# Kernel tuning notes

Hardware: AMD Instinct MI355X
Metric: run time of the kernel (lower is better)

Reference implementation:

```python
import jax, jax.numpy as jnp
import numpy as np

N_TRAIN, N_FEAT, N_HID, ENC = 4096, 64, 256, 256
N_ANTES, ATT_H, MAX_LEN = 2048, 256, 16


def setup_inputs() -> dict:
    key = jax.random.key(0)
    ks = jax.random.split(key, 8)
    s = 0.05
    f32 = jnp.float32
    return {
        "context": jax.random.normal(ks[0], (N_TRAIN, N_FEAT), f32),
        "S": jax.random.uniform(ks[1], (N_TRAIN, N_ANTES), dtype=f32),
        "enc_w1": s * jax.random.normal(ks[2], (N_HID, N_FEAT), f32),
        "enc_b1": jnp.zeros((N_HID,), f32),
        "enc_w2": s * jax.random.normal(ks[3], (ENC, N_HID), f32),
        "enc_b2": jnp.zeros((ENC,), f32),
        "w_ih": s * jax.random.normal(ks[4], (4 * ENC, N_ANTES), f32),
        "w_hh": s * jax.random.normal(ks[5], (4 * ENC, ENC), f32),
        "b_ih": jnp.zeros((4 * ENC,), f32),
        "b_hh": jnp.zeros((4 * ENC,), f32),
        "att_w1": s * jax.random.normal(ks[6], (ATT_H, N_TRAIN + ENC), f32),
        "att_b1": jnp.zeros((ATT_H,), f32),
        "att_w2": s * jax.random.normal(ks[7], (1, ATT_H), f32),
        "att_b2": jnp.zeros((1,), f32),
    }


def _forward(context, S, enc_w1, enc_b1, enc_w2, enc_b2,
             w_ih, w_hh, b_ih, b_hh, att_w1, att_b1, att_w2, att_b2):
    n_train, n_antes = S.shape
    # context encoder: Linear -> ReLU -> Linear, initializes LSTM hidden state
    phi = jax.nn.relu(context @ enc_w1.T + enc_b1) @ enc_w2.T + enc_b2  # [n_train, ENC]
    # attention first layer split: columns [:n_train] act on S.T rows, rest on e_t
    Wa, Wb = att_w1[:, :n_train], att_w1[:, n_train:]
    pre = S.T @ Wa.T  # [n_antes, ATT_H], constant across timesteps
    bias = b_ih + b_hh
    x0 = jnp.ones((n_train, n_antes), S.dtype)

    def step(carry, _):
        h, c, x = carry
        # one LSTM cell step (PyTorch gate order i, f, g, o)
        z = x @ w_ih.T + h @ w_hh.T + bias  # [n_train, 4*ENC]
        i, f, g, o = jnp.split(z, 4, axis=-1)
        c = jax.nn.sigmoid(f) * c + jax.nn.sigmoid(i) * jnp.tanh(g)
        h = jax.nn.sigmoid(o) * jnp.tanh(c)
        e_t = h.mean(axis=0)  # mean over n_train (torch e.mean(1) on [1,n_train,H])
        hid = jax.nn.relu(pre + e_t @ Wb.T + att_b1)  # [n_antes, ATT_H]
        scores = (hid @ att_w2.T + att_b2)[:, 0]      # [n_antes]
        logp = jax.nn.log_softmax(scores, axis=0)
        idx = jnp.argmax(logp)
        # next input: chosen antecedent column broadcast across all antecedents
        x_next = jnp.broadcast_to(S[:, idx][:, None], (n_train, n_antes))
        return (h, c, x_next), logp

    _, d = jax.lax.scan(jax.checkpoint(step), (phi, jnp.zeros_like(phi), x0),
                        None, length=MAX_LEN)
    return d  # [MAX_LEN, n_antes] == torch cat(...).transpose(0, 1)


def reference(context, S, enc_w1, enc_b1, enc_w2, enc_b2,
              w_ih, w_hh, b_ih, b_hh, att_w1, att_b1, att_w2, att_b2):
    return _forward(context, S, enc_w1, enc_b1, enc_w2, enc_b2,
                    w_ih, w_hh, b_ih, b_hh, att_w1, att_b1, att_w2, att_b2)
```

## Files before the change

kernel.cpp:

```cpp
#include <hip/hip_runtime.h>
#include <hip/hip_bf16.h>
#include <math.h>

#define N_TRAIN 4096
#define N_FEAT  64
#define N_HID   256
#define ENC     256
#define N_ANTES 2048
#define ATT_H   256
#define MAX_LEN 16

typedef unsigned int u32;
typedef unsigned short u16;
typedef short short8 __attribute__((ext_vector_type(8)));
typedef float floatx16 __attribute__((ext_vector_type(16)));

__device__ __forceinline__ float fsig(float x)  { return 1.f / (1.f + __expf(-x)); }
__device__ __forceinline__ float ftanh(float x) { return 2.f / (1.f + __expf(-2.f * x)) - 1.f; }

__device__ __forceinline__ u16 f2bf(float x) {
    u32 b = __float_as_uint(x);
    return (u16)((b + 0x7FFFu + ((b >> 16) & 1u)) >> 16);
}
__device__ __forceinline__ float bf2f(u16 h) {
    return __uint_as_float(((u32)h) << 16);
}

__device__ __forceinline__ int kin_of(int l, int j) {
    return ((l >> 5) << 2) + (j & 3) + ((j >> 2) << 3);
}

template <bool RELU>
__global__ __launch_bounds__(256) void gemm_abT(
    const float* __restrict__ A, const float* __restrict__ B,
    const float* __restrict__ bias, float* __restrict__ C,
    int M, int N, int K, int lda, int ldb, int ldc)
{
    __shared__ __align__(16) float As[16][68];
    __shared__ __align__(16) float Bs[16][68];
    const int tid = threadIdx.x;
    const int m0 = blockIdx.x * 64, n0 = blockIdx.y * 64;
    const int tx = tid & 15, ty = tid >> 4;
    const int kl = tid & 15, rl = tid >> 4;
    float acc[4][4] = {};

    for (int k0 = 0; k0 < K; k0 += 16) {
        #pragma unroll
        for (int pp = 0; pp < 4; ++pp) {
            int r = rl + pp * 16;
            As[kl][r] = A[(size_t)(m0 + r) * lda + k0 + kl];
            Bs[kl][r] = B[(size_t)(n0 + r) * ldb + k0 + kl];
        }
        __syncthreads();
        #pragma unroll
        for (int k = 0; k < 16; ++k) {
            float4 av = *(const float4*)&As[k][ty * 4];
            float4 bv = *(const float4*)&Bs[k][tx * 4];
            float a4[4] = {av.x, av.y, av.z, av.w};
            float b4[4] = {bv.x, bv.y, bv.z, bv.w};
            #pragma unroll
            for (int i = 0; i < 4; ++i)
                #pragma unroll
                for (int j = 0; j < 4; ++j)
                    acc[i][j] = fmaf(a4[i], b4[j], acc[i][j]);
        }
        __syncthreads();
    }
    #pragma unroll
    for (int i = 0; i < 4; ++i) {
        int m = m0 + ty * 4 + i;
        #pragma unroll
        for (int j = 0; j < 4; ++j) {
            int n = n0 + tx * 4 + j;
            float v = acc[i][j] + bias[n];
            if (RELU) v = fmaxf(v, 0.f);
            C[(size_t)m * ldc + n] = v;
        }
    }
}

#define KSPLIT 8
__global__ __launch_bounds__(256) void gemm_ab_splitk(
    const float* __restrict__ A, const float* __restrict__ B,
    float* __restrict__ P0, float* __restrict__ P1, float* __restrict__ P2,
    int M, int N, int K, int lda, int ldb, int ldc)
{
    __shared__ __align__(16) float As[16][68];
    __shared__ __align__(16) float Bs[16][64];
    const int tid = threadIdx.x;
    const int m0 = blockIdx.x * 64, n0 = blockIdx.y * 64;
    const int kchunk = K / KSPLIT;
    const int kbeg = blockIdx.z * kchunk, kend = kbeg + kchunk;
    const int tx = tid & 15, ty = tid >> 4;
    const int kl = tid & 15, rl = tid >> 4;
    const int kb = tid >> 6, nb = tid & 63;
    float acc[4][4] = {};

    for (int k0 = kbeg; k0 < kend; k0 += 16) {
        #pragma unroll
        for (int pp = 0; pp < 4; ++pp) {
            As[kl][rl + pp * 16] = A[(size_t)(m0 + rl + pp * 16) * lda + k0 + kl];
            Bs[kb + pp * 4][nb]  = B[(size_t)(k0 + kb + pp * 4) * ldb + n0 + nb];
        }
        __syncthreads();
        #pragma unroll
        for (int k = 0; k < 16; ++k) {
            float4 av = *(const float4*)&As[k][ty * 4];
            float4 bv = *(const float4*)&Bs[k][tx * 4];
            float a4[4] = {av.x, av.y, av.z, av.w};
            float b4[4] = {bv.x, bv.y, bv.z, bv.w};
            #pragma unroll
            for (int i = 0; i < 4; ++i)
                #pragma unroll
                for (int j = 0; j < 4; ++j)
                    acc[i][j] = fmaf(a4[i], b4[j], acc[i][j]);
        }
        __syncthreads();
    }
    const int SZ = ATT_H * N_ANTES;
    const int bz = blockIdx.z;
    float* Cp = (bz < 4) ? P0 + (size_t)bz * SZ
              : (bz < 6) ? P1 + (size_t)(bz - 4) * SZ
                         : P2 + (size_t)(bz - 6) * SZ;
    #pragma unroll
    for (int i = 0; i < 4; ++i)
        #pragma unroll
        for (int j = 0; j < 4; ++j)
            Cp[(size_t)(m0 + ty * 4 + i) * ldc + n0 + tx * 4 + j] = acc[i][j];
}

__global__ __launch_bounds__(256) void k_reduce(
    const float* __restrict__ P0, const float* __restrict__ P1,
    const float* __restrict__ P2, float* __restrict__ preT)
{
    int gid = blockIdx.x * 256 + threadIdx.x;
    const int SZ = ATT_H * N_ANTES;
    float s = ((P0[gid] + P0[gid + SZ]) + (P0[gid + 2 * SZ] + P0[gid + 3 * SZ]))
            + ((P1[gid] + P1[gid + SZ]) + (P2[gid] + P2[gid + SZ]));
    preT[gid] = s;
}

__global__ __launch_bounds__(256) void k_rowsum(const float* __restrict__ w_ih,
                                                float* __restrict__ rowsum)
{
    __shared__ float red[256];
    const int j = blockIdx.x, tid = threadIdx.x;
    float s = 0.f;
    for (int i = tid; i < N_ANTES; i += 256) s += w_ih[(size_t)j * N_ANTES + i];
    red[tid] = s; __syncthreads();
    for (int off = 128; off > 0; off >>= 1) {
        if (tid < off) red[tid] += red[tid + off];
        __syncthreads();
    }
    if (tid == 0) rowsum[j] = red[0];
}

__global__ __launch_bounds__(256) void k_wbT(const float* __restrict__ att_w1,
                                             float* __restrict__ WbT)
{
    int gid = blockIdx.x * 256 + threadIdx.x;
    int j = gid >> 8, k = gid & 255;
    WbT[(size_t)k * 256 + j] = att_w1[(size_t)j * (N_TRAIN + ENC) + N_TRAIN + k];
}

__global__ __launch_bounds__(256) void k_packWf(const float* __restrict__ w_hh,
                                                u16* __restrict__ Wf_hi,
                                                u16* __restrict__ Wf_lo)
{
    int gid = blockIdx.x * 256 + threadIdx.x;
    int j    = gid & 7;
    int l    = (gid >> 3) & 63;
    int kt   = (gid >> 9) & 15;
    int nsub = (gid >> 13) & 1;
    int cb   = gid >> 14;
    int k  = kt * 16 + kin_of(l, j);
    int cc = nsub * 32 + (l & 31);
    int jj = cb * 16 + (cc >> 2);
    int g  = cc & 3;
    int J  = g * 256 + jj;
    float v = w_hh[(size_t)J * 256 + k];
    u16 hi = f2bf(v);
    Wf_hi[gid] = hi;
    Wf_lo[gid] = f2bf(v - bf2f(hi));
}

__global__ __launch_bounds__(256) void k_packHf(const float* __restrict__ h,
                                                u16* __restrict__ Hf_hi,
                                                u16* __restrict__ Hf_lo)
{
    int gid = blockIdx.x * 256 + threadIdx.x;
    int j  = gid & 7;
    int l  = (gid >> 3) & 63;
    int kt = (gid >> 9) & 15;
    int mt = gid >> 13;
    int m = mt * 32 + (l & 31);
    int k = kt * 16 + kin_of(l, j);
    float v = h[(size_t)m * 256 + k];
    u16 hi = f2bf(v);
    Hf_hi[gid] = hi;
    Hf_lo[gid] = f2bf(v - bf2f(hi));
}

__global__ __launch_bounds__(256) void k_zgemm(
    const u16* __restrict__ Hf_hi_r, const u16* __restrict__ Hf_lo_r,
    u16* __restrict__ Hf_hi_w, u16* __restrict__ Hf_lo_w,
    const u16* __restrict__ Wf_hi, const u16* __restrict__ Wf_lo,
    float* __restrict__ c,
    const float* __restrict__ rowsum, const float* __restrict__ b_ih,
    const float* __restrict__ b_hh, const float* __restrict__ S,
    const int* __restrict__ idx_buf, int t, float* __restrict__ e_acc_t)
{
    __shared__ __align__(16) float z_lds[128][68];
    __shared__ float red[256];
    const int tid  = threadIdx.x;
    const int lane = tid & 63;
    const int msub = tid >> 6;
    const int rb = blockIdx.x;
    const int cb = blockIdx.y;
    const int mt = rb * 4 + msub;

    floatx16 acc0 = {0,0,0,0,0,0,0,0,0,0,0,0,0,0,0,0};
    floatx16 acc1 = {0,0,0,0,0,0,0,0,0,0,0,0,0,0,0,0};
    const size_t aoff  = (size_t)mt * 16 * 512 + lane * 8;
    const size_t boff0 = (size_t)(cb * 2 + 0) * 16 * 512 + lane * 8;
    const size_t boff1 = (size_t)(cb * 2 + 1) * 16 * 512 + lane * 8;

    #pragma unroll 4
    for (int kt = 0; kt < 16; ++kt) {
        short8 ahi = *(const short8*)(Hf_hi_r + aoff  + kt * 512);
        short8 alo = *(const short8*)(Hf_lo_r + aoff  + kt * 512);
        short8 b0h = *(const short8*)(Wf_hi   + boff0 + kt * 512);
        short8 b0l = *(const short8*)(Wf_lo   + boff0 + kt * 512);
        short8 b1h = *(const short8*)(Wf_hi   + boff1 + kt * 512);
        short8 b1l = *(const short8*)(Wf_lo   + boff1 + kt * 512);
        acc0 = __builtin_amdgcn_mfma_f32_32x32x16_bf16(ahi, b0h, acc0, 0, 0, 0);
        acc0 = __builtin_amdgcn_mfma_f32_32x32x16_bf16(ahi, b0l, acc0, 0, 0, 0);
        acc0 = __builtin_amdgcn_mfma_f32_32x32x16_bf16(alo, b0h, acc0, 0, 0, 0);
        acc1 = __builtin_amdgcn_mfma_f32_32x32x16_bf16(ahi, b1h, acc1, 0, 0, 0);
        acc1 = __builtin_amdgcn_mfma_f32_32x32x16_bf16(ahi, b1l, acc1, 0, 0, 0);
        acc1 = __builtin_amdgcn_mfma_f32_32x32x16_bf16(alo, b1h, acc1, 0, 0, 0);
    }

    #pragma unroll
    for (int q = 0; q < 16; ++q) {
        int row = msub * 32 + (q & 3) + 8 * (q >> 2) + 4 * (lane >> 5);
        z_lds[row][lane & 31]        = acc0[q];
        z_lds[row][32 + (lane & 31)] = acc1[q];
    }
    __syncthreads();

    const int jj_l = tid & 15, rg = tid >> 4;
    const int Jc = cb * 16 + jj_l;
    float rs[4], bs[4];
    #pragma unroll
    for (int g = 0; g < 4; ++g) {
        int J = g * 256 + Jc;
        rs[g] = rowsum[J];
        bs[g] = b_ih[J] + b_hh[J];
    }
    const int idxp = (t > 0) ? idx_buf[t - 1] : 0;
    float esum = 0.f;
    #pragma unroll
    for (int p = 0; p < 8; ++p) {
        int r = rg * 8 + p;
        int rglob = rb * 128 + r;
        float a = (t > 0) ? S[(size_t)rglob * N_ANTES + idxp] : 1.f;
        float4 z4 = *(const float4*)&z_lds[r][jj_l * 4];
        float zi = z4.x + fmaf(a, rs[0], bs[0]);
        float zf = z4.y + fmaf(a, rs[1], bs[1]);
        float zg = z4.z + fmaf(a, rs[2], bs[2]);
        float zo = z4.w + fmaf(a, rs[3], bs[3]);
        size_t coff = (size_t)rglob * 256 + Jc;
        float cn = fsig(zf) * c[coff] + fsig(zi) * ftanh(zg);
        float hn = fsig(zo) * ftanh(cn);
        c[coff] = cn;
        esum += hn;
        u16 hi = f2bf(hn);
        u16 lo = f2bf(hn - bf2f(hi));
        int mtw    = rglob >> 5;
        int lane_a = (rglob & 31) + 32 * ((Jc >> 2) & 1);
        int ktw    = Jc >> 4;
        int jw     = (Jc & 3) + ((Jc >> 3) & 1) * 4;
        size_t off = (((size_t)mtw * 16 + ktw) * 64 + lane_a) * 8 + jw;
        Hf_hi_w[off] = hi;
        Hf_lo_w[off] = lo;
    }
    red[tid] = esum;
    __syncthreads();
    if (tid < 16) {
        float s = 0.f;
        #pragma unroll
        for (int q = 0; q < 16; ++q) s += red[tid + q * 16];
        atomicAdd(&e_acc_t[Jc - jj_l + tid], s);
    }
}

__global__ __launch_bounds__(256) void k_att(
    const float* __restrict__ preT, const float* __restrict__ e_accum_t,
    const float* __restrict__ WbT, const float* __restrict__ att_b1,
    const float* __restrict__ att_w2, const float* __restrict__ att_b2,
    float* __restrict__ scores, float* __restrict__ out_t,
    int* __restrict__ idx_t, int* __restrict__ cnt)
{
    __shared__ float e_lds[256];
    __shared__ float u[256];
    __shared__ float w2s[256];
    __shared__ float red[256];
    const int tid = threadIdx.x;
    e_lds[tid] = e_accum_t[tid] * (1.f / (float)N_TRAIN);
    w2s[tid] = att_w2[tid];
    __syncthreads();

    float uacc = att_b1[tid];
    for (int k = 0; k < 256; ++k)
        uacc = fmaf(e_lds[k], WbT[(size_t)k * 256 + tid], uacc);
    u[tid] = uacc;
    __syncthreads();

    const int pl = tid & 31, jq = tid >> 5;
    const int p = blockIdx.x * 32 + pl;
    float sc = 0.f;
    #pragma unroll 4
    for (int j = jq; j < 256; j += 8) {
        float v = preT[(size_t)j * N_ANTES + p] + u[j];
        sc = fmaf(fmaxf(v, 0.f), w2s[j], sc);
    }
    red[tid] = sc;
    __syncthreads();
    if (tid < 32) {
        float s = att_b2[0];
        #pragma unroll
        for (int q = 0; q < 8; ++q) s += red[tid + q * 32];
        scores[blockIdx.x * 32 + tid] = s;
    }

    __threadfence();
    __syncthreads();
    __shared__ int is_last;
    if (tid == 0)
        is_last = (atomicAdd(cnt, 1) == (int)gridDim.x - 1);
    __syncthreads();
    if (!is_last) return;
    __threadfence();

    __shared__ float smax[256];
    __shared__ int   sidx[256];
    __shared__ float ssum[256];

    float sv[8];
    #pragma unroll
    for (int i = 0; i < 8; ++i) sv[i] = scores[tid * 8 + i];

    float lmax = -INFINITY; int lidx = 0;
    #pragma unroll
    for (int i = 0; i < 8; ++i)
        if (sv[i] > lmax) { lmax = sv[i]; lidx = tid * 8 + i; }
    smax[tid] = lmax; sidx[tid] = lidx;
    __syncthreads();
    for (int off = 128; off > 0; off >>= 1) {
        if (tid < off) {
            float ov = smax[tid + off]; int oi = sidx[tid + off];
            if (ov > smax[tid] || (ov == smax[tid] && oi < sidx[tid])) {
                smax[tid] = ov; sidx[tid] = oi;
            }
        }
        __syncthreads();
    }
    const float gmax = smax[0];
    const int gidx = sidx[0];

    float lsum = 0.f;
    #pragma unroll
    for (int i = 0; i < 8; ++i) lsum += __expf(sv[i] - gmax);
    ssum[tid] = lsum;
    __syncthreads();
    for (int off = 128; off > 0; off >>= 1) {
        if (tid < off) ssum[tid] += ssum[tid + off];
        __syncthreads();
    }
    const float lse = gmax + logf(ssum[0]);

    #pragma unroll
    for (int i = 0; i < 8; ++i)
        out_t[tid * 8 + i] = sv[i] - lse;
    if (tid == 0) {
        idx_t[0] = gidx;
        *cnt = 0;
    }
}

extern "C" void kernel_launch(void* const* d_in, const int* in_sizes, int n_in,
                              void* d_out, int out_size, void* d_ws, size_t ws_size,
                              hipStream_t stream)
{
    (void)in_sizes; (void)n_in; (void)out_size; (void)ws_size;
    const float* context = (const float*)d_in[0];
    const float* S       = (const float*)d_in[1];
    const float* enc_w1  = (const float*)d_in[2];
    const float* enc_b1  = (const float*)d_in[3];
    const float* enc_w2  = (const float*)d_in[4];
    const float* enc_b2  = (const float*)d_in[5];
    const float* w_ih    = (const float*)d_in[6];
    const float* w_hh    = (const float*)d_in[7];
    const float* b_ih    = (const float*)d_in[8];
    const float* b_hh    = (const float*)d_in[9];
    const float* att_w1  = (const float*)d_in[10];
    const float* att_b1  = (const float*)d_in[11];
    const float* att_w2  = (const float*)d_in[12];
    const float* att_b2  = (const float*)d_in[13];
    float* out = (float*)d_out;
    float* ws  = (float*)d_ws;

    float* h_fp32 = ws;
    float* c      = ws + 1048576;
    float* hid1   = ws + 2097152;
    float* preT   = ws + 3145728;
    float* P2     = ws + 3670016;
    u16* Hf_hi1 = (u16*)(ws + 0);
    u16* Hf_lo1 = (u16*)(ws + 524288);
    u16* Hf_hi0 = (u16*)(ws + 2097152);
    u16* Hf_lo0 = (u16*)(ws + 2621440);
    u16* Wf_hi  = (u16*)(ws + 3670016);
    u16* Wf_lo  = (u16*)(ws + 3801088);
    int*   cnt    = (int*)(ws + 4718592);
    float* rowsum = ws + 4984832;
    float* e_acc  = ws + 4985856;
    float* scores = ws + 4989952;
    float* WbT    = ws + 4992000;
    int*   idxbuf = (int*)(ws + 5057536);

    k_rowsum<<<1024, 256, 0, stream>>>(w_ih, rowsum);
    k_wbT<<<256, 256, 0, stream>>>(att_w1, WbT);

    dim3 g3(ATT_H / 64, N_ANTES / 64, KSPLIT);
    gemm_ab_splitk<<<g3, 256, 0, stream>>>(att_w1, S, ws, hid1, P2,
                                           ATT_H, N_ANTES, N_TRAIN,
                                           N_TRAIN + ENC, N_ANTES, N_ANTES);
    k_reduce<<<(ATT_H * N_ANTES) / 256, 256, 0, stream>>>(ws, hid1, P2, preT);

    k_packWf<<<1024, 256, 0, stream>>>(w_hh, Wf_hi, Wf_lo);
    hipMemsetAsync(c, 0, (size_t)N_TRAIN * ENC * sizeof(float), stream);
    hipMemsetAsync(e_acc, 0, (size_t)MAX_LEN * ENC * sizeof(float), stream);
    hipMemsetAsync(cnt, 0, sizeof(int), stream);

    dim3 g1(N_TRAIN / 64, N_HID / 64);
    gemm_abT<true><<<g1, 256, 0, stream>>>(context, enc_w1, enc_b1, hid1,
                                           N_TRAIN, N_HID, N_FEAT, N_FEAT, N_FEAT, N_HID);
    dim3 g2(N_TRAIN / 64, ENC / 64);
    gemm_abT<false><<<g2, 256, 0, stream>>>(hid1, enc_w2, enc_b2, h_fp32,
                                            N_TRAIN, ENC, N_HID, N_HID, N_HID, ENC);
    k_packHf<<<4096, 256, 0, stream>>>(h_fp32, Hf_hi0, Hf_lo0);

    dim3 gz(32, 16);
    for (int t = 0; t < MAX_LEN; ++t) {
        const u16 *hr, *lr; u16 *hw, *lw;
        if ((t & 1) == 0) { hr = Hf_hi0; lr = Hf_lo0; hw = Hf_hi1; lw = Hf_lo1; }
        else              { hr = Hf_hi1; lr = Hf_lo1; hw = Hf_hi0; lw = Hf_lo0; }
        k_zgemm<<<gz, 256, 0, stream>>>(hr, lr, hw, lw, Wf_hi, Wf_lo, c,
                                        rowsum, b_ih, b_hh, S, idxbuf, t,
                                        e_acc + t * 256);
        k_att<<<N_ANTES / 32, 256, 0, stream>>>(preT, e_acc + t * 256, WbT,
                                                att_b1, att_w2, att_b2, scores,
                                                out + t * N_ANTES, idxbuf + t, cnt);
    }
}
```

Baseline: 725.3 us.

## Compute attention precompute GEMM with split-bf16 MFMA instead of FP32 split-K

Replaces the FP32 SIMT split-K GEMM for pre = att_w1[:, :n_train] @ S with an MFMA kernel that uses a 3-term bf16 hi/lo split to keep roughly FP32 accuracy. att_w1 is pre-packed into the MFMA fragment layout, and S is split on the fly. The split-K factor drops from 8 to 4, so the reduce kernel reads fewer partials. It adds a pack kernel and strided global reads of S without LDS staging, and the hi/lo split is a truncation-based approximation of FP32.

```diff
diff --git a/kernel.cpp b/kernel.cpp
--- a/kernel.cpp
+++ b/kernel.cpp
@@ -24,6 +24,12 @@
 }
 __device__ __forceinline__ float bf2f(u16 h) {
     return __uint_as_float(((u32)h) << 16);
+}
+__device__ __forceinline__ void split_bf(float v, u16& hi, u16& lo) {
+    u32 b = __float_as_uint(v);
+    hi = (u16)(b >> 16);
+    float r = v - __uint_as_float(b & 0xFFFF0000u);
+    lo = (u16)(__float_as_uint(r) >> 16);
 }
 
 __device__ __forceinline__ int kin_of(int l, int j) {
@@ -79,67 +85,6 @@
     }
 }
 
-#define KSPLIT 8
-__global__ __launch_bounds__(256) void gemm_ab_splitk(
-    const float* __restrict__ A, const float* __restrict__ B,
-    float* __restrict__ P0, float* __restrict__ P1, float* __restrict__ P2,
-    int M, int N, int K, int lda, int ldb, int ldc)
-{
-    __shared__ __align__(16) float As[16][68];
-    __shared__ __align__(16) float Bs[16][64];
-    const int tid = threadIdx.x;
-    const int m0 = blockIdx.x * 64, n0 = blockIdx.y * 64;
-    const int kchunk = K / KSPLIT;
-    const int kbeg = blockIdx.z * kchunk, kend = kbeg + kchunk;
-    const int tx = tid & 15, ty = tid >> 4;
-    const int kl = tid & 15, rl = tid >> 4;
-    const int kb = tid >> 6, nb = tid & 63;
-    float acc[4][4] = {};
-
-    for (int k0 = kbeg; k0 < kend; k0 += 16) {
-        #pragma unroll
-        for (int pp = 0; pp < 4; ++pp) {
-            As[kl][rl + pp * 16] = A[(size_t)(m0 + rl + pp * 16) * lda + k0 + kl];
-            Bs[kb + pp * 4][nb]  = B[(size_t)(k0 + kb + pp * 4) * ldb + n0 + nb];
-        }
-        __syncthreads();
-        #pragma unroll
-        for (int k = 0; k < 16; ++k) {
-            float4 av = *(const float4*)&As[k][ty * 4];
-            float4 bv = *(const float4*)&Bs[k][tx * 4];
-            float a4[4] = {av.x, av.y, av.z, av.w};
-            float b4[4] = {bv.x, bv.y, bv.z, bv.w};
-            #pragma unroll
-            for (int i = 0; i < 4; ++i)
-                #pragma unroll
-                for (int j = 0; j < 4; ++j)
-                    acc[i][j] = fmaf(a4[i], b4[j], acc[i][j]);
-        }
-        __syncthreads();
-    }
-    const int SZ = ATT_H * N_ANTES;
-    const int bz = blockIdx.z;
-    float* Cp = (bz < 4) ? P0 + (size_t)bz * SZ
-              : (bz < 6) ? P1 + (size_t)(bz - 4) * SZ
-                         : P2 + (size_t)(bz - 6) * SZ;
-    #pragma unroll
-    for (int i = 0; i < 4; ++i)
-        #pragma unroll
-        for (int j = 0; j < 4; ++j)
-            Cp[(size_t)(m0 + ty * 4 + i) * ldc + n0 + tx * 4 + j] = acc[i][j];
-}
-
-__global__ __launch_bounds__(256) void k_reduce(
-    const float* __restrict__ P0, const float* __restrict__ P1,
-    const float* __restrict__ P2, float* __restrict__ preT)
-{
-    int gid = blockIdx.x * 256 + threadIdx.x;
-    const int SZ = ATT_H * N_ANTES;
-    float s = ((P0[gid] + P0[gid + SZ]) + (P0[gid + 2 * SZ] + P0[gid + 3 * SZ]))
-            + ((P1[gid] + P1[gid + SZ]) + (P2[gid] + P2[gid + SZ]));
-    preT[gid] = s;
-}
-
 __global__ __launch_bounds__(256) void k_rowsum(const float* __restrict__ w_ih,
                                                 float* __restrict__ rowsum)
 {
@@ -161,6 +106,90 @@
     int gid = blockIdx.x * 256 + threadIdx.x;
     int j = gid >> 8, k = gid & 255;
     WbT[(size_t)k * 256 + j] = att_w1[(size_t)j * (N_TRAIN + ENC) + N_TRAIN + k];
+}
+
+__global__ __launch_bounds__(256) void k_packAf(const float* __restrict__ att_w1,
+                                                u16* __restrict__ Af_hi,
+                                                u16* __restrict__ Af_lo)
+{
+    int gid = blockIdx.x * 256 + threadIdx.x;
+    int j  = gid & 7;
+    int l  = (gid >> 3) & 63;
+    int kt = (gid >> 9) & 255;
+    int mt = gid >> 17;
+    int m = mt * 32 + (l & 31);
+    int k = kt * 16 + kin_of(l, j);
+    float v = att_w1[(size_t)m * (N_TRAIN + ENC) + k];
+    u16 hi, lo; split_bf(v, hi, lo);
+    Af_hi[gid] = hi;
+    Af_lo[gid] = lo;
+}
+
+#define PSPLIT 4
+__global__ __launch_bounds__(256) void k_gemm_preT(
+    const u16* __restrict__ Af_hi, const u16* __restrict__ Af_lo,
+    const float* __restrict__ S, float* __restrict__ P)
+{
+    const int tid = threadIdx.x, lane = tid & 63, w = tid >> 6;
+    const int kz = blockIdx.x;
+    const int np = blockIdx.y;
+    const int p0 = np * 64;
+    const int nb = p0 + (lane & 31);
+    const int kb = 4 * (lane >> 5);
+    floatx16 acc[2][2] = {};
+
+    const int kt_beg = kz * 64, kt_end = kt_beg + 64;
+    #pragma unroll 2
+    for (int kt = kt_beg; kt < kt_end; ++kt) {
+        short8 ahi[2], alo[2], bhi[2], blo[2];
+        #pragma unroll
+        for (int mi = 0; mi < 2; ++mi) {
+            size_t ao = (((size_t)(w * 2 + mi) * 256 + kt) * 64 + lane) * 8;
+            ahi[mi] = *(const short8*)(Af_hi + ao);
+            alo[mi] = *(const short8*)(Af_lo + ao);
+        }
+        #pragma unroll
+        for (int ni = 0; ni < 2; ++ni) {
+            #pragma unroll
+            for (int j = 0; j < 8; ++j) {
+                int k = kt * 16 + kb + (j & 3) + 8 * (j >> 2);
+                float v = S[(size_t)k * N_ANTES + nb + ni * 32];
+                u16 hi, lo; split_bf(v, hi, lo);
+                bhi[ni][j] = (short)hi;
+                blo[ni][j] = (short)lo;
+            }
+        }
+        #pragma unroll
+        for (int mi = 0; mi < 2; ++mi)
+            #pragma unroll
+            for (int ni = 0; ni < 2; ++ni) {
+                acc[mi][ni] = __builtin_amdgcn_mfma_f32_32x32x16_bf16(
+                    ahi[mi], bhi[ni], acc[mi][ni], 0, 0, 0);
+                acc[mi][ni] = __builtin_amdgcn_mfma_f32_32x32x16_bf16(
+                    ahi[mi], blo[ni], acc[mi][ni], 0, 0, 0);
+                acc[mi][ni] = __builtin_amdgcn_mfma_f32_32x32x16_bf16(
+                    alo[mi], bhi[ni], acc[mi][ni], 0, 0, 0);
+            }
+    }
+
+    float* Pk = P + (size_t)kz * (ATT_H * N_ANTES);
+    #pragma unroll
+    for (int mi = 0; mi < 2; ++mi)
+        #pragma unroll
+        for (int ni = 0; ni < 2; ++ni)
+            #pragma unroll
+            for (int q = 0; q < 16; ++q) {
+                int row = w * 64 + mi * 32 + (q & 3) + 8 * (q >> 2) + 4 * (lane >> 5);
+                Pk[(size_t)row * N_ANTES + p0 + ni * 32 + (lane & 31)] = acc[mi][ni][q];
+            }
+}
+
+__global__ __launch_bounds__(256) void k_reduce4(const float* __restrict__ P,
+                                                 float* __restrict__ preT)
+{
+    int gid = blockIdx.x * 256 + threadIdx.x;
+    const int SZ = ATT_H * N_ANTES;
+    preT[gid] = (P[gid] + P[gid + SZ]) + (P[gid + 2 * SZ] + P[gid + 3 * SZ]);
 }
 
 __global__ __launch_bounds__(256) void k_packWf(const float* __restrict__ w_hh,
@@ -411,11 +440,13 @@
     float* out = (float*)d_out;
     float* ws  = (float*)d_ws;
 
+    float* P      = ws;
     float* h_fp32 = ws;
     float* c      = ws + 1048576;
     float* hid1   = ws + 2097152;
     float* preT   = ws + 3145728;
-    float* P2     = ws + 3670016;
+    u16* Af_hi  = (u16*)(ws + 2097152);
+    u16* Af_lo  = (u16*)(ws + 2621440);
     u16* Hf_hi1 = (u16*)(ws + 0);
     u16* Hf_lo1 = (u16*)(ws + 524288);
     u16* Hf_hi0 = (u16*)(ws + 2097152);
@@ -431,14 +462,13 @@
 
     k_rowsum<<<1024, 256, 0, stream>>>(w_ih, rowsum);
     k_wbT<<<256, 256, 0, stream>>>(att_w1, WbT);
-
-    dim3 g3(ATT_H / 64, N_ANTES / 64, KSPLIT);
-    gemm_ab_splitk<<<g3, 256, 0, stream>>>(att_w1, S, ws, hid1, P2,
-                                           ATT_H, N_ANTES, N_TRAIN,
-                                           N_TRAIN + ENC, N_ANTES, N_ANTES);
-    k_reduce<<<(ATT_H * N_ANTES) / 256, 256, 0, stream>>>(ws, hid1, P2, preT);
-
     k_packWf<<<1024, 256, 0, stream>>>(w_hh, Wf_hi, Wf_lo);
+
+    k_packAf<<<4096, 256, 0, stream>>>(att_w1, Af_hi, Af_lo);
+    dim3 gp(PSPLIT, N_ANTES / 64);
+    k_gemm_preT<<<gp, 256, 0, stream>>>(Af_hi, Af_lo, S, P);
+    k_reduce4<<<(ATT_H * N_ANTES) / 256, 256, 0, stream>>>(P, preT);
+
     hipMemsetAsync(c, 0, (size_t)N_TRAIN * ENC * sizeof(float), stream);
     hipMemsetAsync(e_acc, 0, (size_t)MAX_LEN * ENC * sizeof(float), stream);
     hipMemsetAsync(cnt, 0, sizeof(int), stream);
```

Result: no change. 723.0 us (-0.3%).
